# Optimization experiments

Hardware: AMD Instinct MI355X
Metric: run time of the kernel (lower is better)

Reference implementation:

```python
import jax, jax.numpy as jnp
import numpy as np
import math

NEIGHBOR_RADIUS = 30.0

def _masked_softmax(logits, mask, axis):
    # mask: bool, True = keep; all-masked rows return zeros
    p = jax.nn.softmax(jnp.where(mask, logits, -1e9), axis=axis) * mask.astype(logits.dtype)
    return p / jnp.clip(jnp.sum(p, axis=axis, keepdims=True), 1e-9, None)

def _forward(agents_state, agents_mask, map_polylines, map_poly_mask,
             map_poly_type, map_tl_status, map_on_route,
             pm_w1, pm_b1, pm_w2, pm_b2, type_emb, tl_emb, route_emb,
             mo_w1, mo_b1, mo_w2, mo_b2,
             ae_w1, ae_b1, ae_w2, ae_b2, ae_w3, ae_b3,
             mr_w1, mr_b1, mr_w2, mr_b2,
             nr_w1, nr_b1, nr_w2, nr_b2,
             to_w1, to_b1, to_w2, to_b2):
    relu = jax.nn.relu
    a_mask = (agents_mask > 0.5).astype(agents_state.dtype)   # (B,N,T)
    a_feat = agents_state[..., :5]
    # ---- map polyline node encoder ----
    h = relu(map_polylines @ pm_w1 + pm_b1)                   # (B,M,L,H)
    h = relu(h @ pm_w2 + pm_b2)
    h = h.max(axis=2)                                         # (B,M,H) max-pool over points
    t_idx = jnp.clip(map_poly_type, 0, type_emb.shape[0] - 1)
    s_idx = jnp.clip(map_tl_status, 0, tl_emb.shape[0] - 1)
    r_idx = jnp.clip(map_on_route, 0, route_emb.shape[0] - 1)
    h = h + type_emb[t_idx] + tl_emb[s_idx] + route_emb[r_idx]
    h = relu(h @ mo_w1 + mo_b1) @ mo_w2 + mo_b2
    map_mask = map_poly_mask > 0.5                            # (B,M) bool
    map_node = h * map_mask[..., None].astype(h.dtype)        # (B,M,D)
    map_center = map_polylines.mean(axis=2)                   # (B,M,2)
    # ---- agent state encoder ----
    a = relu(a_feat @ ae_w1 + ae_b1)
    a = relu(a @ ae_w2 + ae_b2)
    a_emb = (a @ ae_w3 + ae_b3) * a_mask[..., None]           # (B,N,T,D)
    D = a_emb.shape[-1]
    # ---- agent -> map attention ----
    agent_pos = a_feat[..., 0:2]
    rel = map_center[:, None, None, :, :] - agent_pos[:, :, :, None, :]  # (B,N,T,M,2)
    dist = jnp.linalg.norm(rel, axis=-1, keepdims=True)
    rel_feat = jnp.concatenate([rel, dist], axis=-1)          # (B,N,T,M,3)
    rel_score = (relu(rel_feat @ mr_w1 + mr_b1) @ mr_w2 + mr_b2)[..., 0]  # (B,N,T,M)
    dot = jnp.einsum('bntd,bmd->bntm', a_emb, map_node) / math.sqrt(D)
    score_mask = jnp.broadcast_to(map_mask[:, None, None, :], dot.shape)
    attn = _masked_softmax(dot + rel_score, score_mask, axis=-1)
    map_ctx = jnp.einsum('bntm,bmd->bntd', attn, map_node)    # (B,N,T,D)
    # ---- neighbor graph attention ----
    pos = a_feat[..., 0:2]
    vel = a_feat[..., 3:5]
    pos_j = jnp.transpose(pos, (0, 2, 1, 3))                  # (B,T,N,2)
    vel_j = jnp.transpose(vel, (0, 2, 1, 3))
    rel_pos = pos_j[:, None, :, :, :] - pos[:, :, :, None, :] # (B,N,T,N,2) = p_j - p_i
    rel_vel = vel_j[:, None, :, :, :] - vel[:, :, :, None, :]
    dist_ij = jnp.linalg.norm(rel_pos, axis=-1, keepdims=True)
    rel_ij = jnp.concatenate([rel_pos, rel_vel, dist_ij], axis=-1)        # (B,N,T,N,5)
    nbr_score = (relu(rel_ij @ nr_w1 + nr_b1) @ nr_w2 + nr_b2)[..., 0]    # (B,N,T,N)
    am_b = agents_mask > 0.5
    valid_i = am_b[..., None]                                 # (B,N,T,1)
    valid_j = jnp.transpose(am_b, (0, 2, 1))[:, None, :, :]   # (B,1,T,N)
    N = pos.shape[1]
    not_self = ~jnp.eye(N, dtype=bool)[None, :, None, :]      # (1,N,1,N)
    nbr_mask = valid_i & valid_j & (dist_ij[..., 0] <= NEIGHBOR_RADIUS) & not_self
    dot_n = jnp.einsum('bitd,bjtd->bitj', a_emb, a_emb) / math.sqrt(D)
    w_n = _masked_softmax(dot_n + nbr_score, nbr_mask, axis=-1)
    nbr_ctx = jnp.einsum('bitj,bjtd->bitd', w_n, a_emb)       # (B,N,T,D)
    # ---- tau head ----
    tau = jnp.concatenate([a_emb, map_ctx, nbr_ctx], axis=-1)
    tau = relu(tau @ to_w1 + to_b1) @ to_w2 + to_b2
    return tau * a_mask[..., None]

def setup_inputs() -> dict:
    key = jax.random.key(0)
    B, N, T, M, L = 2, 32, 32, 256, 20
    H, D, TAU = 128, 128, 64
    ks = jax.random.split(key, 32)
    def f(i, shp):
        return jax.random.normal(ks[i], shp, jnp.float32) * 0.05
    inp = {}
    inp['agents_state'] = jax.random.normal(ks[0], (B, N, T, 5), jnp.float32) * jnp.array([50., 50., 1., 5., 5.], jnp.float32)
    inp['agents_mask'] = jnp.ones((B, N, T), jnp.float32)
    inp['map_polylines'] = jax.random.normal(ks[1], (B, M, L, 2), jnp.float32) * 50.0
    inp['map_poly_mask'] = jnp.ones((B, M), jnp.float32)
    inp['map_poly_type'] = jax.random.randint(ks[2], (B, M), 0, 4)
    inp['map_tl_status'] = jax.random.randint(ks[3], (B, M), 0, 8)
    inp['map_on_route'] = jax.random.randint(ks[4], (B, M), 0, 2)
    inp['pm_w1'] = f(5, (2, H));  inp['pm_b1'] = jnp.zeros((H,), jnp.float32)
    inp['pm_w2'] = f(6, (H, H)); inp['pm_b2'] = jnp.zeros((H,), jnp.float32)
    inp['type_emb'] = f(7, (4, H)); inp['tl_emb'] = f(8, (8, H)); inp['route_emb'] = f(9, (2, H))
    inp['mo_w1'] = f(10, (H, H)); inp['mo_b1'] = jnp.zeros((H,), jnp.float32)
    inp['mo_w2'] = f(11, (H, D)); inp['mo_b2'] = jnp.zeros((D,), jnp.float32)
    inp['ae_w1'] = f(12, (5, H)); inp['ae_b1'] = jnp.zeros((H,), jnp.float32)
    inp['ae_w2'] = f(13, (H, H)); inp['ae_b2'] = jnp.zeros((H,), jnp.float32)
    inp['ae_w3'] = f(14, (H, D)); inp['ae_b3'] = jnp.zeros((D,), jnp.float32)
    inp['mr_w1'] = f(15, (3, H)); inp['mr_b1'] = jnp.zeros((H,), jnp.float32)
    inp['mr_w2'] = f(16, (H, 1)); inp['mr_b2'] = jnp.zeros((1,), jnp.float32)
    inp['nr_w1'] = f(17, (5, H)); inp['nr_b1'] = jnp.zeros((H,), jnp.float32)
    inp['nr_w2'] = f(18, (H, 1)); inp['nr_b2'] = jnp.zeros((1,), jnp.float32)
    inp['to_w1'] = f(19, (3 * D, H)); inp['to_b1'] = jnp.zeros((H,), jnp.float32)
    inp['to_w2'] = f(20, (H, TAU)); inp['to_b2'] = jnp.zeros((TAU,), jnp.float32)
    return inp

def reference(agents_state, agents_mask, map_polylines, map_poly_mask,
              map_poly_type, map_tl_status, map_on_route,
              pm_w1, pm_b1, pm_w2, pm_b2, type_emb, tl_emb, route_emb,
              mo_w1, mo_b1, mo_w2, mo_b2,
              ae_w1, ae_b1, ae_w2, ae_b2, ae_w3, ae_b3,
              mr_w1, mr_b1, mr_w2, mr_b2,
              nr_w1, nr_b1, nr_w2, nr_b2,
              to_w1, to_b1, to_w2, to_b2):
    return _forward(agents_state, agents_mask, map_polylines, map_poly_mask,
                    map_poly_type, map_tl_status, map_on_route,
                    pm_w1, pm_b1, pm_w2, pm_b2, type_emb, tl_emb, route_emb,
                    mo_w1, mo_b1, mo_w2, mo_b2,
                    ae_w1, ae_b1, ae_w2, ae_b2, ae_w3, ae_b3,
                    mr_w1, mr_b1, mr_w2, mr_b2,
                    nr_w1, nr_b1, nr_w2, nr_b2,
                    to_w1, to_b1, to_w2, to_b2)
```

## Files before the change

kernel.cpp:

```cpp
#include <hip/hip_runtime.h>
#include <hip/hip_bf16.h>

#define Bb 2
#define Nn 32
#define Tt 32
#define Mm 256
#define Ll 20
#define Hh 128
#define Dd 128
#define TAUu 64
#define RSQRT_D 0.08838834764831843f

__device__ __forceinline__ float rlane(float v, int l) {
    return __int_as_float(__builtin_amdgcn_readlane(__float_as_int(v), l));
}

__global__ __launch_bounds__(128) void k_map(
    const float* __restrict__ poly, const float* __restrict__ pmask,
    const int* __restrict__ ptype, const int* __restrict__ ptl, const int* __restrict__ proute,
    const float* __restrict__ pm_w1, const float* __restrict__ pm_b1,
    const float* __restrict__ pm_w2, const float* __restrict__ pm_b2,
    const float* __restrict__ type_emb, const float* __restrict__ tl_emb, const float* __restrict__ route_emb,
    const float* __restrict__ mo_w1, const float* __restrict__ mo_b1,
    const float* __restrict__ mo_w2, const float* __restrict__ mo_b2,
    float* __restrict__ map_node, float* __restrict__ map_nodeT, float* __restrict__ map_center)
{
    int bm = blockIdx.x;
    int b  = bm >> 8, m = bm & 255;
    int h  = threadIdx.x;
    int lam = h & 63, wv = h >> 6;
    int obase = ((wv ^ 1) << 6) + lam;
    __shared__ float xch[Ll][Hh];

    const float* pp = poly + bm * (Ll*2);
    float w1x = pm_w1[h], w1y = pm_w1[Hh+h], b1v = pm_b1[h];
    float h1r[Ll];
    #pragma unroll
    for (int l = 0; l < Ll; ++l) {
        float xl = pp[2*l], yl = pp[2*l+1];
        h1r[l] = fmaxf(fmaf(w1x, xl, fmaf(w1y, yl, b1v)), 0.f);
    }
    #pragma unroll
    for (int l = 0; l < Ll; ++l) xch[l][h] = h1r[l];
    __syncthreads();
    float lo[Ll], hi[Ll];
    #pragma unroll
    for (int l = 0; l < Ll; ++l) {
        float o = xch[l][obase];
        lo[l] = wv ? o : h1r[l];
        hi[l] = wv ? h1r[l] : o;
    }
    float b2v = pm_b2[h];
    float acc[Ll];
    #pragma unroll
    for (int l = 0; l < Ll; ++l) acc[l] = b2v;
    #pragma unroll
    for (int k = 0; k < 64; ++k) {
        float w = pm_w2[k*Hh + h];
        #pragma unroll
        for (int l = 0; l < Ll; ++l) acc[l] = fmaf(rlane(lo[l], k), w, acc[l]);
    }
    #pragma unroll
    for (int k = 0; k < 64; ++k) {
        float w = pm_w2[(64+k)*Hh + h];
        #pragma unroll
        for (int l = 0; l < Ll; ++l) acc[l] = fmaf(rlane(hi[l], k), w, acc[l]);
    }
    float mx = 0.f;
    #pragma unroll
    for (int l = 0; l < Ll; ++l) mx = fmaxf(mx, acc[l]);

    int ti = min(max(ptype[bm], 0), 3);
    int si = min(max(ptl[bm], 0), 7);
    int ri = min(max(proute[bm], 0), 1);
    float hval = mx + type_emb[ti*Hh+h] + tl_emb[si*Hh+h] + route_emb[ri*Hh+h];

    __syncthreads();
    xch[0][h] = hval;
    __syncthreads();
    {
        float o = xch[0][obase];
        float l1 = wv ? o : hval, h1 = wv ? hval : o;
        float a1 = mo_b1[h];
        #pragma unroll
        for (int k = 0; k < 64; ++k) a1 = fmaf(rlane(l1, k), mo_w1[k*Hh + h], a1);
        #pragma unroll
        for (int k = 0; k < 64; ++k) a1 = fmaf(rlane(h1, k), mo_w1[(64+k)*Hh + h], a1);
        hval = fmaxf(a1, 0.f);
    }
    __syncthreads();
    xch[0][h] = hval;
    __syncthreads();
    float val;
    {
        float o = xch[0][obase];
        float l1 = wv ? o : hval, h1 = wv ? hval : o;
        float a2 = mo_b2[h];
        #pragma unroll
        for (int k = 0; k < 64; ++k) a2 = fmaf(rlane(l1, k), mo_w2[k*Dd + h], a2);
        #pragma unroll
        for (int k = 0; k < 64; ++k) a2 = fmaf(rlane(h1, k), mo_w2[(64+k)*Dd + h], a2);
        val = a2;
    }
    float mk = (pmask[bm] > 0.5f) ? 1.f : 0.f;
    val *= mk;
    map_node[bm*Dd + h] = val;
    map_nodeT[(b*Dd + h)*Mm + m] = val;
    if (h == 0) {
        float sx = 0.f, sy = 0.f;
        #pragma unroll
        for (int l = 0; l < Ll; ++l) { sx += pp[2*l]; sy += pp[2*l+1]; }
        map_center[bm*2+0] = sx / (float)Ll;
        map_center[bm*2+1] = sy / (float)Ll;
    }
}

__global__ __launch_bounds__(128) void k_agent(
    const float* __restrict__ astate, const float* __restrict__ amask,
    const float* __restrict__ ae_w1, const float* __restrict__ ae_b1,
    const float* __restrict__ ae_w2, const float* __restrict__ ae_b2,
    const float* __restrict__ ae_w3, const float* __restrict__ ae_b3,
    float* __restrict__ a_emb)
{
    int r0 = blockIdx.x * 4;
    int h  = threadIdx.x;
    int lam = h & 63, wv = h >> 6;
    int obase = ((wv ^ 1) << 6) + lam;
    __shared__ float xch[4][Hh];

    float w1[5];
    #pragma unroll
    for (int k = 0; k < 5; ++k) w1[k] = ae_w1[k*Hh + h];
    float b1v = ae_b1[h];
    float a1[4];
    #pragma unroll
    for (int r = 0; r < 4; ++r) {
        const float* st = astate + (r0+r)*5;
        float a = b1v;
        #pragma unroll
        for (int k = 0; k < 5; ++k) a = fmaf(w1[k], st[k], a);
        a1[r] = fmaxf(a, 0.f);
    }
    #pragma unroll
    for (int r = 0; r < 4; ++r) xch[r][h] = a1[r];
    __syncthreads();
    float lo[4], hi[4];
    #pragma unroll
    for (int r = 0; r < 4; ++r) {
        float o = xch[r][obase];
        lo[r] = wv ? o : a1[r];
        hi[r] = wv ? a1[r] : o;
    }
    float b2v = ae_b2[h];
    float ac[4] = {b2v, b2v, b2v, b2v};
    #pragma unroll
    for (int k = 0; k < 64; ++k) {
        float w = ae_w2[k*Hh + h];
        #pragma unroll
        for (int r = 0; r < 4; ++r) ac[r] = fmaf(rlane(lo[r], k), w, ac[r]);
    }
    #pragma unroll
    for (int k = 0; k < 64; ++k) {
        float w = ae_w2[(64+k)*Hh + h];
        #pragma unroll
        for (int r = 0; r < 4; ++r) ac[r] = fmaf(rlane(hi[r], k), w, ac[r]);
    }
    #pragma unroll
    for (int r = 0; r < 4; ++r) a1[r] = fmaxf(ac[r], 0.f);
    __syncthreads();
    #pragma unroll
    for (int r = 0; r < 4; ++r) xch[r][h] = a1[r];
    __syncthreads();
    #pragma unroll
    for (int r = 0; r < 4; ++r) {
        float o = xch[r][obase];
        lo[r] = wv ? o : a1[r];
        hi[r] = wv ? a1[r] : o;
    }
    float b3v = ae_b3[h];
    #pragma unroll
    for (int r = 0; r < 4; ++r) ac[r] = b3v;
    #pragma unroll
    for (int k = 0; k < 64; ++k) {
        float w = ae_w3[k*Dd + h];
        #pragma unroll
        for (int r = 0; r < 4; ++r) ac[r] = fmaf(rlane(lo[r], k), w, ac[r]);
    }
    #pragma unroll
    for (int k = 0; k < 64; ++k) {
        float w = ae_w3[(64+k)*Dd + h];
        #pragma unroll
        for (int r = 0; r < 4; ++r) ac[r] = fmaf(rlane(hi[r], k), w, ac[r]);
    }
    #pragma unroll
    for (int r = 0; r < 4; ++r) {
        float mk = (amask[r0+r] > 0.5f) ? 1.f : 0.f;
        a_emb[(r0+r)*Dd + h] = ac[r] * mk;
    }
}

__global__ __launch_bounds__(256) void k_fused(
    const float* __restrict__ astate, const float* __restrict__ amask,
    const float* __restrict__ pmask,
    const float* __restrict__ a_emb, const float* __restrict__ map_node,
    const float* __restrict__ map_nodeT, const float* __restrict__ map_center,
    const float* __restrict__ mr_w1, const float* __restrict__ mr_b1,
    const float* __restrict__ mr_w2, const float* __restrict__ mr_b2,
    const float* __restrict__ nr_w1, const float* __restrict__ nr_b1,
    const float* __restrict__ nr_w2, const float* __restrict__ nr_b2,
    const float* __restrict__ to_w1, const float* __restrict__ to_b1,
    const float* __restrict__ to_w2, const float* __restrict__ to_b2,
    float* __restrict__ out)
{
    int r0 = blockIdx.x * 4;
    int b  = r0 >> 10;
    int i  = (r0 >> 5) & 31;
    int t0 = r0 & 31;
    int tid = threadIdx.x;
    int lam = tid & 63, wv = tid >> 6;

    __shared__ float tau[4][3*Dd];
    __shared__ float lg4[4][Mm];
    __shared__ float p4[Mm][4];
    __shared__ float ctxp[4][512];
    __shared__ float w1n_s[5*Hh];
    __shared__ float b1n_s[Hh];
    __shared__ float w2n_s[Hh];
    __shared__ float jd[4][Nn][5];
    __shared__ float lgn[4][Nn];
    __shared__ float p4n[Nn][4];
    __shared__ float g1s[4][Hh];

    for (int q = tid; q < 512; q += 256) tau[q>>7][q&127] = a_emb[(r0 + (q>>7))*Dd + (q&127)];
    for (int q = tid; q < 5*Hh; q += 256) w1n_s[q] = nr_w1[q];
    if (tid < Hh) { b1n_s[tid] = nr_b1[tid]; w2n_s[tid] = nr_w2[tid]; }
    if (tid < 128) {
        int rr = tid >> 5, j = tid & 31;
        int rj = (b*Nn + j)*Tt + t0 + rr;
        jd[rr][j][0] = astate[rj*5+0];
        jd[rr][j][1] = astate[rj*5+1];
        jd[rr][j][2] = astate[rj*5+3];
        jd[rr][j][3] = astate[rj*5+4];
        jd[rr][j][4] = amask[rj];
    }
    __syncthreads();

    {
        int m = tid;
        float cx = map_center[(b*Mm+m)*2+0];
        float cy = map_center[(b*Mm+m)*2+1];
        float rx[4], ry[4], dv[4], sA[4], dt[4];
        float b2c = mr_b2[0];
        #pragma unroll
        for (int r = 0; r < 4; ++r) {
            float px = astate[(r0+r)*5+0];
            float py = astate[(r0+r)*5+1];
            rx[r] = cx - px; ry[r] = cy - py;
            dv[r] = sqrtf(rx[r]*rx[r] + ry[r]*ry[r]);
            sA[r] = b2c; dt[r] = 0.f;
        }
        #pragma unroll 4
        for (int k = 0; k < Hh; ++k) {
            float wa = mr_w1[k], wb = mr_w1[Hh+k], wc = mr_w1[2*Hh+k];
            float bb = mr_b1[k], w2 = mr_w2[k];
            #pragma unroll
            for (int r = 0; r < 4; ++r) {
                float t1 = fmaf(rx[r], wa, fmaf(ry[r], wb, fmaf(dv[r], wc, bb)));
                t1 = fmaxf(t1, 0.f);
                sA[r] = fmaf(t1, w2, sA[r]);
            }
        }
        #pragma unroll 4
        for (int d = 0; d < Dd; ++d) {
            float v = map_nodeT[(b*Dd + d)*Mm + m];
            #pragma unroll
            for (int r = 0; r < 4; ++r)
                dt[r] = fmaf(v, a_emb[(r0+r)*Dd + d], dt[r]);
        }
        bool mk = pmask[b*Mm+m] > 0.5f;
        #pragma unroll
        for (int r = 0; r < 4; ++r)
            lg4[r][m] = mk ? fmaf(dt[r], RSQRT_D, sA[r]) : -1e30f;
    }
    __syncthreads();

    {
        float x0 = lg4[wv][lam], x1 = lg4[wv][64+lam], x2 = lg4[wv][128+lam], x3 = lg4[wv][192+lam];
        float mxv = fmaxf(fmaxf(x0,x1), fmaxf(x2,x3));
        for (int off = 32; off; off >>= 1) mxv = fmaxf(mxv, __shfl_xor(mxv, off));
        float e0 = (x0 > -1e29f) ? expf(x0-mxv) : 0.f;
        float e1 = (x1 > -1e29f) ? expf(x1-mxv) : 0.f;
        float e2 = (x2 > -1e29f) ? expf(x2-mxv) : 0.f;
        float e3 = (x3 > -1e29f) ? expf(x3-mxv) : 0.f;
        float sm = e0+e1+e2+e3;
        for (int off = 32; off; off >>= 1) sm += __shfl_xor(sm, off);
        float inv = 1.f / fmaxf(sm, 1e-9f);
        p4[lam][wv]     = e0*inv;
        p4[64+lam][wv]  = e1*inv;
        p4[128+lam][wv] = e2*inv;
        p4[192+lam][wv] = e3*inv;
    }
    __syncthreads();

    {
        int m0 = wv * 64;
        float4 pv = *(const float4*)&p4[m0 + lam][0];
        float pr0 = pv.x, pr1 = pv.y, pr2 = pv.z, pr3 = pv.w;
        float a00=0.f,a01=0.f,a10=0.f,a11=0.f,a20=0.f,a21=0.f,a30=0.f,a31=0.f;
        #pragma unroll
        for (int mm = 0; mm < 64; ++mm) {
            const float* np = map_node + (b*Mm + m0 + mm)*Dd;
            float v0 = np[lam], v1 = np[64+lam];
            float s0 = rlane(pr0, mm), s1 = rlane(pr1, mm), s2 = rlane(pr2, mm), s3 = rlane(pr3, mm);
            a00 = fmaf(s0, v0, a00); a01 = fmaf(s0, v1, a01);
            a10 = fmaf(s1, v0, a10); a11 = fmaf(s1, v1, a11);
            a20 = fmaf(s2, v0, a20); a21 = fmaf(s2, v1, a21);
            a30 = fmaf(s3, v0, a30); a31 = fmaf(s3, v1, a31);
        }
        ctxp[wv][0*Dd + lam] = a00; ctxp[wv][0*Dd + 64+lam] = a01;
        ctxp[wv][1*Dd + lam] = a10; ctxp[wv][1*Dd + 64+lam] = a11;
        ctxp[wv][2*Dd + lam] = a20; ctxp[wv][2*Dd + 64+lam] = a21;
        ctxp[wv][3*Dd + lam] = a30; ctxp[wv][3*Dd + 64+lam] = a31;
    }
    __syncthreads();
    for (int q = tid; q < 512; q += 256) {
        float s = ctxp[0][q] + ctxp[1][q] + ctxp[2][q] + ctxp[3][q];
        tau[q>>7][Dd + (q&127)] = s;
    }
    __syncthreads();

    {
        int j = tid >> 3, c = tid & 7;
        float b2c = nr_b2[0];
        float rpx[4], rpy[4], rvx[4], rvy[4], dd[4], am[4], ad[4];
        #pragma unroll
        for (int r = 0; r < 4; ++r) {
            float pxi = astate[(r0+r)*5+0], pyi = astate[(r0+r)*5+1];
            float vxi = astate[(r0+r)*5+3], vyi = astate[(r0+r)*5+4];
            rpx[r] = jd[r][j][0] - pxi; rpy[r] = jd[r][j][1] - pyi;
            rvx[r] = jd[r][j][2] - vxi; rvy[r] = jd[r][j][3] - vyi;
            dd[r]  = sqrtf(rpx[r]*rpx[r] + rpy[r]*rpy[r]);
            am[r] = 0.f; ad[r] = 0.f;
        }
        #pragma unroll
        for (int u = 0; u < 16; ++u) {
            int hh = (u<<3) + c;
            float wA = w1n_s[hh], wB = w1n_s[Hh+hh], wC = w1n_s[2*Hh+hh];
            float wD = w1n_s[3*Hh+hh], wE = w1n_s[4*Hh+hh];
            float bb = b1n_s[hh], w2 = w2n_s[hh];
            #pragma unroll
            for (int r = 0; r < 4; ++r) {
                float t1 = fmaf(rpx[r], wA, fmaf(rpy[r], wB, fmaf(rvx[r], wC,
                           fmaf(rvy[r], wD, fmaf(dd[r], wE, bb)))));
                t1 = fmaxf(t1, 0.f);
                am[r] = fmaf(t1, w2, am[r]);
                float ejv = a_emb[((size_t)((b*Nn + j)*Tt + t0 + r))*Dd + hh];
                ad[r] = fmaf(tau[r][hh], ejv, ad[r]);
            }
        }
        #pragma unroll
        for (int r = 0; r < 4; ++r) {
            am[r] += __shfl_xor(am[r], 1); ad[r] += __shfl_xor(ad[r], 1);
            am[r] += __shfl_xor(am[r], 2); ad[r] += __shfl_xor(ad[r], 2);
            am[r] += __shfl_xor(am[r], 4); ad[r] += __shfl_xor(ad[r], 4);
        }
        if (c == 0) {
            #pragma unroll
            for (int r = 0; r < 4; ++r) {
                bool vi = amask[r0+r] > 0.5f;
                bool vj = jd[r][j][4] > 0.5f;
                bool ok = vi && vj && (dd[r] <= 30.0f) && (j != i);
                lgn[r][j] = ok ? fmaf(ad[r], RSQRT_D, b2c + am[r]) : -1e30f;
            }
        }
    }
    __syncthreads();

    {
        float x = (lam < Nn) ? lgn[wv][lam] : -1e30f;
        float mxv = x;
        for (int off = 32; off; off >>= 1) mxv = fmaxf(mxv, __shfl_xor(mxv, off));
        float e = (x > -1e29f) ? expf(x - mxv) : 0.f;
        float sm = e;
        for (int off = 32; off; off >>= 1) sm += __shfl_xor(sm, off);
        float inv = 1.f / fmaxf(sm, 1e-9f);
        if (lam < Nn) p4n[lam][wv] = e * inv;
    }
    __syncthreads();

    {
        int d = tid & 127, hf = tid >> 7;
        float ac[4] = {0.f,0.f,0.f,0.f};
        #pragma unroll
        for (int jj = 0; jj < 16; ++jj) {
            int j2 = (hf<<4) + jj;
            float4 pv = *(const float4*)&p4n[j2][0];
            size_t base = (size_t)((b*Nn + j2)*Tt + t0);
            float v0 = a_emb[(base+0)*Dd + d];
            float v1 = a_emb[(base+1)*Dd + d];
            float v2 = a_emb[(base+2)*Dd + d];
            float v3 = a_emb[(base+3)*Dd + d];
            ac[0] = fmaf(pv.x, v0, ac[0]);
            ac[1] = fmaf(pv.y, v1, ac[1]);
            ac[2] = fmaf(pv.z, v2, ac[2]);
            ac[3] = fmaf(pv.w, v3, ac[3]);
        }
        if (hf == 1) {
            #pragma unroll
            for (int r = 0; r < 4; ++r) ctxp[0][r*Dd + d] = ac[r];
        }
        __syncthreads();
        if (hf == 0) {
            #pragma unroll
            for (int r = 0; r < 4; ++r) tau[r][2*Dd + d] = ac[r] + ctxp[0][r*Dd + d];
        }
    }
    __syncthreads();

    {
        int h = tid & 127, rp = tid >> 7;
        float ta[6], tb[6];
        #pragma unroll
        for (int c = 0; c < 6; ++c) {
            ta[c] = tau[rp][c*64 + lam];
            tb[c] = tau[rp+2][c*64 + lam];
        }
        float acc0 = 0.f, acc1 = 0.f;
        #pragma unroll
        for (int c = 0; c < 6; ++c) {
            #pragma unroll
            for (int kk = 0; kk < 64; ++kk) {
                float w = to_w1[(c*64+kk)*Hh + h];
                acc0 = fmaf(rlane(ta[c], kk), w, acc0);
                acc1 = fmaf(rlane(tb[c], kk), w, acc1);
            }
        }
        float bv = to_b1[h];
        g1s[rp][h]   = fmaxf(acc0 + bv, 0.f);
        g1s[rp+2][h] = fmaxf(acc1 + bv, 0.f);
    }
    __syncthreads();

    {
        float ga = g1s[wv][lam], gb = g1s[wv][64+lam];
        float acc = to_b2[lam];
        #pragma unroll
        for (int kk = 0; kk < 64; ++kk)
            acc = fmaf(rlane(ga, kk), to_w2[kk*TAUu + lam], acc);
        #pragma unroll
        for (int kk = 0; kk < 64; ++kk)
            acc = fmaf(rlane(gb, kk), to_w2[(64+kk)*TAUu + lam], acc);
        float mk = (amask[r0+wv] > 0.5f) ? 1.f : 0.f;
        out[(r0+wv)*TAUu + lam] = acc * mk;
    }
}

extern "C" void kernel_launch(void* const* d_in, const int* in_sizes, int n_in,
                              void* d_out, int out_size, void* d_ws, size_t ws_size,
                              hipStream_t stream) {
    const float* agents_state  = (const float*)d_in[0];
    const float* agents_mask   = (const float*)d_in[1];
    const float* map_polylines = (const float*)d_in[2];
    const float* map_poly_mask = (const float*)d_in[3];
    const int*   map_poly_type = (const int*)d_in[4];
    const int*   map_tl_status = (const int*)d_in[5];
    const int*   map_on_route  = (const int*)d_in[6];
    const float* pm_w1 = (const float*)d_in[7];
    const float* pm_b1 = (const float*)d_in[8];
    const float* pm_w2 = (const float*)d_in[9];
    const float* pm_b2 = (const float*)d_in[10];
    const float* type_emb  = (const float*)d_in[11];
    const float* tl_emb    = (const float*)d_in[12];
    const float* route_emb = (const float*)d_in[13];
    const float* mo_w1 = (const float*)d_in[14];
    const float* mo_b1 = (const float*)d_in[15];
    const float* mo_w2 = (const float*)d_in[16];
    const float* mo_b2 = (const float*)d_in[17];
    const float* ae_w1 = (const float*)d_in[18];
    const float* ae_b1 = (const float*)d_in[19];
    const float* ae_w2 = (const float*)d_in[20];
    const float* ae_b2 = (const float*)d_in[21];
    const float* ae_w3 = (const float*)d_in[22];
    const float* ae_b3 = (const float*)d_in[23];
    const float* mr_w1 = (const float*)d_in[24];
    const float* mr_b1 = (const float*)d_in[25];
    const float* mr_w2 = (const float*)d_in[26];
    const float* mr_b2 = (const float*)d_in[27];
    const float* nr_w1 = (const float*)d_in[28];
    const float* nr_b1 = (const float*)d_in[29];
    const float* nr_w2 = (const float*)d_in[30];
    const float* nr_b2 = (const float*)d_in[31];
    const float* to_w1 = (const float*)d_in[32];
    const float* to_b1 = (const float*)d_in[33];
    const float* to_w2 = (const float*)d_in[34];
    const float* to_b2 = (const float*)d_in[35];

    float* ws = (float*)d_ws;
    float* map_node   = ws;
    float* map_nodeT  = ws + 65536;
    float* map_center = ws + 131072;
    float* a_emb      = ws + 132096;

    float* out = (float*)d_out;

    k_map<<<Bb*Mm, 128, 0, stream>>>(map_polylines, map_poly_mask,
        map_poly_type, map_tl_status, map_on_route,
        pm_w1, pm_b1, pm_w2, pm_b2, type_emb, tl_emb, route_emb,
        mo_w1, mo_b1, mo_w2, mo_b2, map_node, map_nodeT, map_center);

    k_agent<<<Bb*Nn*Tt/4, 128, 0, stream>>>(agents_state, agents_mask,
        ae_w1, ae_b1, ae_w2, ae_b2, ae_w3, ae_b3, a_emb);

    k_fused<<<Bb*Nn*Tt/4, 256, 0, stream>>>(agents_state, agents_mask,
        map_poly_mask, a_emb, map_node, map_nodeT, map_center,
        mr_w1, mr_b1, mr_w2, mr_b2,
        nr_w1, nr_b1, nr_w2, nr_b2,
        to_w1, to_b1, to_w2, to_b2, out);
}
```

Before: 210.1 us.

## Restructure pipeline into three kernels with precomputed first-layer projections

Replaces the map/agent/fused kernel trio with three new kernels. The first merges the map and agent encoders into one launch and splits each K reduction across waves. The encoders now also precompute the linear parts of the relation MLPs (map-center and agent-position projections), plus transposed agent embeddings and position tables. The second kernel computes map and neighbor attention in separate block ranges, and the third runs the trajectory output MLP. The aim is to remove redundant per-pair first-layer work and raise parallelism, at the cost of more workspace traffic and an extra launch.

```diff
diff --git a/kernel.cpp b/kernel.cpp
--- a/kernel.cpp
+++ b/kernel.cpp
@@ -1,21 +1,12 @@
 #include <hip/hip_runtime.h>
-#include <hip/hip_bf16.h>
-
-#define Bb 2
-#define Nn 32
-#define Tt 32
-#define Mm 256
-#define Ll 20
-#define Hh 128
-#define Dd 128
-#define TAUu 64
+
 #define RSQRT_D 0.08838834764831843f
 
-__device__ __forceinline__ float rlane(float v, int l) {
+__device__ __forceinline__ float rl(float v, int l) {
     return __int_as_float(__builtin_amdgcn_readlane(__float_as_int(v), l));
 }
 
-__global__ __launch_bounds__(128) void k_map(
+__global__ __launch_bounds__(256) void k_p1(
     const float* __restrict__ poly, const float* __restrict__ pmask,
     const int* __restrict__ ptype, const int* __restrict__ ptl, const int* __restrict__ proute,
     const float* __restrict__ pm_w1, const float* __restrict__ pm_b1,
@@ -23,436 +14,432 @@
     const float* __restrict__ type_emb, const float* __restrict__ tl_emb, const float* __restrict__ route_emb,
     const float* __restrict__ mo_w1, const float* __restrict__ mo_b1,
     const float* __restrict__ mo_w2, const float* __restrict__ mo_b2,
-    float* __restrict__ map_node, float* __restrict__ map_nodeT, float* __restrict__ map_center)
-{
-    int bm = blockIdx.x;
-    int b  = bm >> 8, m = bm & 255;
-    int h  = threadIdx.x;
-    int lam = h & 63, wv = h >> 6;
-    int obase = ((wv ^ 1) << 6) + lam;
-    __shared__ float xch[Ll][Hh];
-
-    const float* pp = poly + bm * (Ll*2);
-    float w1x = pm_w1[h], w1y = pm_w1[Hh+h], b1v = pm_b1[h];
-    float h1r[Ll];
-    #pragma unroll
-    for (int l = 0; l < Ll; ++l) {
-        float xl = pp[2*l], yl = pp[2*l+1];
-        h1r[l] = fmaxf(fmaf(w1x, xl, fmaf(w1y, yl, b1v)), 0.f);
-    }
-    #pragma unroll
-    for (int l = 0; l < Ll; ++l) xch[l][h] = h1r[l];
-    __syncthreads();
-    float lo[Ll], hi[Ll];
-    #pragma unroll
-    for (int l = 0; l < Ll; ++l) {
-        float o = xch[l][obase];
-        lo[l] = wv ? o : h1r[l];
-        hi[l] = wv ? h1r[l] : o;
-    }
-    float b2v = pm_b2[h];
-    float acc[Ll];
-    #pragma unroll
-    for (int l = 0; l < Ll; ++l) acc[l] = b2v;
-    #pragma unroll
-    for (int k = 0; k < 64; ++k) {
-        float w = pm_w2[k*Hh + h];
-        #pragma unroll
-        for (int l = 0; l < Ll; ++l) acc[l] = fmaf(rlane(lo[l], k), w, acc[l]);
-    }
-    #pragma unroll
-    for (int k = 0; k < 64; ++k) {
-        float w = pm_w2[(64+k)*Hh + h];
-        #pragma unroll
-        for (int l = 0; l < Ll; ++l) acc[l] = fmaf(rlane(hi[l], k), w, acc[l]);
-    }
-    float mx = 0.f;
-    #pragma unroll
-    for (int l = 0; l < Ll; ++l) mx = fmaxf(mx, acc[l]);
-
-    int ti = min(max(ptype[bm], 0), 3);
-    int si = min(max(ptl[bm], 0), 7);
-    int ri = min(max(proute[bm], 0), 1);
-    float hval = mx + type_emb[ti*Hh+h] + tl_emb[si*Hh+h] + route_emb[ri*Hh+h];
-
-    __syncthreads();
-    xch[0][h] = hval;
-    __syncthreads();
-    {
-        float o = xch[0][obase];
-        float l1 = wv ? o : hval, h1 = wv ? hval : o;
-        float a1 = mo_b1[h];
-        #pragma unroll
-        for (int k = 0; k < 64; ++k) a1 = fmaf(rlane(l1, k), mo_w1[k*Hh + h], a1);
-        #pragma unroll
-        for (int k = 0; k < 64; ++k) a1 = fmaf(rlane(h1, k), mo_w1[(64+k)*Hh + h], a1);
-        hval = fmaxf(a1, 0.f);
-    }
-    __syncthreads();
-    xch[0][h] = hval;
-    __syncthreads();
-    float val;
-    {
-        float o = xch[0][obase];
-        float l1 = wv ? o : hval, h1 = wv ? hval : o;
-        float a2 = mo_b2[h];
-        #pragma unroll
-        for (int k = 0; k < 64; ++k) a2 = fmaf(rlane(l1, k), mo_w2[k*Dd + h], a2);
-        #pragma unroll
-        for (int k = 0; k < 64; ++k) a2 = fmaf(rlane(h1, k), mo_w2[(64+k)*Dd + h], a2);
-        val = a2;
-    }
-    float mk = (pmask[bm] > 0.5f) ? 1.f : 0.f;
-    val *= mk;
-    map_node[bm*Dd + h] = val;
-    map_nodeT[(b*Dd + h)*Mm + m] = val;
-    if (h == 0) {
-        float sx = 0.f, sy = 0.f;
-        #pragma unroll
-        for (int l = 0; l < Ll; ++l) { sx += pp[2*l]; sy += pp[2*l+1]; }
-        map_center[bm*2+0] = sx / (float)Ll;
-        map_center[bm*2+1] = sy / (float)Ll;
-    }
-}
-
-__global__ __launch_bounds__(128) void k_agent(
+    const float* __restrict__ mr_w1, const float* __restrict__ mr_b1,
     const float* __restrict__ astate, const float* __restrict__ amask,
     const float* __restrict__ ae_w1, const float* __restrict__ ae_b1,
     const float* __restrict__ ae_w2, const float* __restrict__ ae_b2,
     const float* __restrict__ ae_w3, const float* __restrict__ ae_b3,
-    float* __restrict__ a_emb)
+    const float* __restrict__ nr_w1, const float* __restrict__ nr_b1,
+    float* __restrict__ map_node, float* __restrict__ map_nodeT,
+    float* __restrict__ cm, float* __restrict__ center,
+    float* __restrict__ a_emb, float* __restrict__ aT,
+    float* __restrict__ q2, float* __restrict__ qn, float* __restrict__ posT)
 {
-    int r0 = blockIdx.x * 4;
-    int h  = threadIdx.x;
-    int lam = h & 63, wv = h >> 6;
-    int obase = ((wv ^ 1) << 6) + lam;
-    __shared__ float xch[4][Hh];
-
-    float w1[5];
-    #pragma unroll
-    for (int k = 0; k < 5; ++k) w1[k] = ae_w1[k*Hh + h];
-    float b1v = ae_b1[h];
-    float a1[4];
-    #pragma unroll
-    for (int r = 0; r < 4; ++r) {
-        const float* st = astate + (r0+r)*5;
-        float a = b1v;
-        #pragma unroll
-        for (int k = 0; k < 5; ++k) a = fmaf(w1[k], st[k], a);
-        a1[r] = fmaxf(a, 0.f);
-    }
-    #pragma unroll
-    for (int r = 0; r < 4; ++r) xch[r][h] = a1[r];
-    __syncthreads();
-    float lo[4], hi[4];
-    #pragma unroll
-    for (int r = 0; r < 4; ++r) {
-        float o = xch[r][obase];
-        lo[r] = wv ? o : a1[r];
-        hi[r] = wv ? a1[r] : o;
-    }
-    float b2v = ae_b2[h];
-    float ac[4] = {b2v, b2v, b2v, b2v};
-    #pragma unroll
-    for (int k = 0; k < 64; ++k) {
-        float w = ae_w2[k*Hh + h];
-        #pragma unroll
-        for (int r = 0; r < 4; ++r) ac[r] = fmaf(rlane(lo[r], k), w, ac[r]);
-    }
-    #pragma unroll
-    for (int k = 0; k < 64; ++k) {
-        float w = ae_w2[(64+k)*Hh + h];
-        #pragma unroll
-        for (int r = 0; r < 4; ++r) ac[r] = fmaf(rlane(hi[r], k), w, ac[r]);
-    }
-    #pragma unroll
-    for (int r = 0; r < 4; ++r) a1[r] = fmaxf(ac[r], 0.f);
-    __syncthreads();
-    #pragma unroll
-    for (int r = 0; r < 4; ++r) xch[r][h] = a1[r];
-    __syncthreads();
-    #pragma unroll
-    for (int r = 0; r < 4; ++r) {
-        float o = xch[r][obase];
-        lo[r] = wv ? o : a1[r];
-        hi[r] = wv ? a1[r] : o;
-    }
-    float b3v = ae_b3[h];
-    #pragma unroll
-    for (int r = 0; r < 4; ++r) ac[r] = b3v;
-    #pragma unroll
-    for (int k = 0; k < 64; ++k) {
-        float w = ae_w3[k*Dd + h];
-        #pragma unroll
-        for (int r = 0; r < 4; ++r) ac[r] = fmaf(rlane(lo[r], k), w, ac[r]);
-    }
-    #pragma unroll
-    for (int k = 0; k < 64; ++k) {
-        float w = ae_w3[(64+k)*Dd + h];
-        #pragma unroll
-        for (int r = 0; r < 4; ++r) ac[r] = fmaf(rlane(hi[r], k), w, ac[r]);
-    }
-    #pragma unroll
-    for (int r = 0; r < 4; ++r) {
-        float mk = (amask[r0+r] > 0.5f) ? 1.f : 0.f;
-        a_emb[(r0+r)*Dd + h] = ac[r] * mk;
+    int tid = threadIdx.x;
+    int lam = tid & 63;
+    __shared__ float red[20][128];
+    __shared__ float xch[128];
+
+    if (blockIdx.x < 512) {
+        int bm = blockIdx.x;
+        int b = bm >> 8, m = bm & 255;
+        int h = tid & 127, lp = tid >> 7;
+        int pidx = bm*40 + lam; if (pidx > 20479) pidx = 20479;
+        float ptreg = poly[pidx];
+        int x = lp*64 + lam;
+        float w1x = pm_w1[x], w1y = pm_w1[128+x], b1v = pm_b1[x];
+        float h1r[20];
+        #pragma unroll
+        for (int l = 0; l < 20; ++l) {
+            float xl = rl(ptreg, 2*l), yl = rl(ptreg, 2*l+1);
+            h1r[l] = fmaxf(fmaf(w1x, xl, fmaf(w1y, yl, b1v)), 0.f);
+        }
+        float acc[20];
+        #pragma unroll
+        for (int l = 0; l < 20; ++l) acc[l] = 0.f;
+        #pragma unroll
+        for (int kk = 0; kk < 64; ++kk) {
+            float w = pm_w2[(lp*64+kk)*128 + h];
+            #pragma unroll
+            for (int l = 0; l < 20; ++l) acc[l] = fmaf(rl(h1r[l], kk), w, acc[l]);
+        }
+        if (lp == 1) {
+            #pragma unroll
+            for (int l = 0; l < 20; ++l) red[l][h] = acc[l];
+        }
+        __syncthreads();
+        if (lp == 0) {
+            float mx = -1e30f;
+            #pragma unroll
+            for (int l = 0; l < 20; ++l) mx = fmaxf(mx, acc[l] + red[l][h]);
+            mx = fmaxf(mx + pm_b2[h], 0.f);
+            int ti = min(max(ptype[bm],0),3);
+            int si = min(max(ptl[bm],0),7);
+            int ri = min(max(proute[bm],0),1);
+            xch[h] = mx + type_emb[ti*128+h] + tl_emb[si*128+h] + route_emb[ri*128+h];
+        }
+        __syncthreads();
+        float src = xch[lp*64 + lam];
+        float a1p = 0.f;
+        #pragma unroll
+        for (int kk = 0; kk < 64; ++kk)
+            a1p = fmaf(rl(src, kk), mo_w1[(lp*64+kk)*128 + h], a1p);
+        if (lp == 1) red[0][h] = a1p;
+        __syncthreads();
+        if (lp == 0) {
+            float a1v = fmaxf(a1p + red[0][h] + mo_b1[h], 0.f);
+            red[1][h] = a1v;
+        }
+        __syncthreads();
+        float src2 = red[1][lp*64 + lam];
+        float a2p = 0.f;
+        #pragma unroll
+        for (int kk = 0; kk < 64; ++kk)
+            a2p = fmaf(rl(src2, kk), mo_w2[(lp*64+kk)*128 + h], a2p);
+        if (lp == 1) red[2][h] = a2p;
+        __syncthreads();
+        float sx = 0.f, sy = 0.f;
+        #pragma unroll
+        for (int l = 0; l < 20; ++l) { sx += rl(ptreg, 2*l); sy += rl(ptreg, 2*l+1); }
+        sx *= 0.05f; sy *= 0.05f;
+        if (lp == 0) {
+            float val = a2p + red[2][h] + mo_b2[h];
+            float mk = (pmask[bm] > 0.5f) ? 1.f : 0.f;
+            val *= mk;
+            map_node[bm*128 + h] = val;
+            map_nodeT[(b*128+h)*256 + m] = val;
+            cm[(b*128+h)*256 + m] = fmaf(sx, mr_w1[h], fmaf(sy, mr_w1[128+h], mr_b1[h]));
+            if (h == 0) { center[bm*2+0] = sx; center[bm*2+1] = sy; }
+        }
+    } else {
+        int qw = (blockIdx.x - 512)*4 + (tid >> 6);
+        int r0b = qw * 4;
+        int aidx = r0b*5 + lam; if (aidx > 10239) aidx = 10239;
+        float streg = astate[aidx];
+        float w1l[5], w1h[5];
+        #pragma unroll
+        for (int c = 0; c < 5; ++c) { w1l[c] = ae_w1[c*128+lam]; w1h[c] = ae_w1[c*128+64+lam]; }
+        float b1l = ae_b1[lam], b1h = ae_b1[64+lam];
+        float a1lo[4], a1hi[4];
+        #pragma unroll
+        for (int r = 0; r < 4; ++r) {
+            float px = rl(streg, r*5+0), py = rl(streg, r*5+1), pz = rl(streg, r*5+2);
+            float vx = rl(streg, r*5+3), vy = rl(streg, r*5+4);
+            float lo = b1l, hi = b1h;
+            lo = fmaf(px,w1l[0],lo); hi = fmaf(px,w1h[0],hi);
+            lo = fmaf(py,w1l[1],lo); hi = fmaf(py,w1h[1],hi);
+            lo = fmaf(pz,w1l[2],lo); hi = fmaf(pz,w1h[2],hi);
+            lo = fmaf(vx,w1l[3],lo); hi = fmaf(vx,w1h[3],hi);
+            lo = fmaf(vy,w1l[4],lo); hi = fmaf(vy,w1h[4],hi);
+            a1lo[r] = fmaxf(lo, 0.f); a1hi[r] = fmaxf(hi, 0.f);
+        }
+        float c0[4], c1[4];
+        {
+            float b2l = ae_b2[lam], b2h = ae_b2[64+lam];
+            #pragma unroll
+            for (int r = 0; r < 4; ++r) { c0[r] = b2l; c1[r] = b2h; }
+        }
+        #pragma unroll
+        for (int k = 0; k < 64; ++k) {
+            float wl = ae_w2[k*128+lam], wh = ae_w2[k*128+64+lam];
+            #pragma unroll
+            for (int r = 0; r < 4; ++r) { float xv = rl(a1lo[r], k); c0[r]=fmaf(xv,wl,c0[r]); c1[r]=fmaf(xv,wh,c1[r]); }
+        }
+        #pragma unroll
+        for (int k = 0; k < 64; ++k) {
+            float wl = ae_w2[(64+k)*128+lam], wh = ae_w2[(64+k)*128+64+lam];
+            #pragma unroll
+            for (int r = 0; r < 4; ++r) { float xv = rl(a1hi[r], k); c0[r]=fmaf(xv,wl,c0[r]); c1[r]=fmaf(xv,wh,c1[r]); }
+        }
+        #pragma unroll
+        for (int r = 0; r < 4; ++r) { a1lo[r] = fmaxf(c0[r],0.f); a1hi[r] = fmaxf(c1[r],0.f); }
+        {
+            float b3l = ae_b3[lam], b3h = ae_b3[64+lam];
+            #pragma unroll
+            for (int r = 0; r < 4; ++r) { c0[r] = b3l; c1[r] = b3h; }
+        }
+        #pragma unroll
+        for (int k = 0; k < 64; ++k) {
+            float wl = ae_w3[k*128+lam], wh = ae_w3[k*128+64+lam];
+            #pragma unroll
+            for (int r = 0; r < 4; ++r) { float xv = rl(a1lo[r], k); c0[r]=fmaf(xv,wl,c0[r]); c1[r]=fmaf(xv,wh,c1[r]); }
+        }
+        #pragma unroll
+        for (int k = 0; k < 64; ++k) {
+            float wl = ae_w3[(64+k)*128+lam], wh = ae_w3[(64+k)*128+64+lam];
+            #pragma unroll
+            for (int r = 0; r < 4; ++r) { float xv = rl(a1hi[r], k); c0[r]=fmaf(xv,wl,c0[r]); c1[r]=fmaf(xv,wh,c1[r]); }
+        }
+        float nA_l = nr_w1[lam],     nA_h = nr_w1[64+lam];
+        float nB_l = nr_w1[128+lam], nB_h = nr_w1[192+lam];
+        float nC_l = nr_w1[256+lam], nC_h = nr_w1[320+lam];
+        float nD_l = nr_w1[384+lam], nD_h = nr_w1[448+lam];
+        float nb_l = nr_b1[lam],     nb_h = nr_b1[64+lam];
+        #pragma unroll
+        for (int r = 0; r < 4; ++r) {
+            int rr = r0b + r;
+            float mk = (amask[rr] > 0.5f) ? 1.f : 0.f;
+            float e0 = c0[r]*mk, e1 = c1[r]*mk;
+            int bb = rr >> 10, nn = (rr >> 5) & 31, tt = rr & 31;
+            int bt = bb*32 + tt;
+            a_emb[rr*128 + lam]    = e0;
+            a_emb[rr*128 + 64+lam] = e1;
+            aT[(bt*128 + lam)*32 + nn]    = e0;
+            aT[(bt*128 + 64+lam)*32 + nn] = e1;
+            float px = rl(streg, r*5+0), py = rl(streg, r*5+1);
+            float vx = rl(streg, r*5+3), vy = rl(streg, r*5+4);
+            float ql = fmaf(px,nA_l,fmaf(py,nB_l,fmaf(vx,nC_l, vy*nD_l)));
+            float qh = fmaf(px,nA_h,fmaf(py,nB_h,fmaf(vx,nC_h, vy*nD_h)));
+            qn[rr*128 + lam]    = ql;
+            qn[rr*128 + 64+lam] = qh;
+            q2[(bt*128 + lam)*32 + nn]    = ql + nb_l;
+            q2[(bt*128 + 64+lam)*32 + nn] = qh + nb_h;
+            if (lam == 0) {
+                posT[(bt*5+0)*32+nn] = px;
+                posT[(bt*5+1)*32+nn] = py;
+                posT[(bt*5+2)*32+nn] = vx;
+                posT[(bt*5+3)*32+nn] = vy;
+                posT[(bt*5+4)*32+nn] = amask[rr];
+            }
+        }
     }
 }
 
-__global__ __launch_bounds__(256) void k_fused(
-    const float* __restrict__ astate, const float* __restrict__ amask,
-    const float* __restrict__ pmask,
+__global__ __launch_bounds__(256) void k_p2(
+    const float* __restrict__ astate, const float* __restrict__ pmask,
     const float* __restrict__ a_emb, const float* __restrict__ map_node,
-    const float* __restrict__ map_nodeT, const float* __restrict__ map_center,
-    const float* __restrict__ mr_w1, const float* __restrict__ mr_b1,
-    const float* __restrict__ mr_w2, const float* __restrict__ mr_b2,
-    const float* __restrict__ nr_w1, const float* __restrict__ nr_b1,
-    const float* __restrict__ nr_w2, const float* __restrict__ nr_b2,
+    const float* __restrict__ map_nodeT, const float* __restrict__ center,
+    const float* __restrict__ cm,
+    const float* __restrict__ mr_w1, const float* __restrict__ mr_w2, const float* __restrict__ mr_b2,
+    const float* __restrict__ qn, const float* __restrict__ q2,
+    const float* __restrict__ aT, const float* __restrict__ posT,
+    const float* __restrict__ nr_w1, const float* __restrict__ nr_w2, const float* __restrict__ nr_b2,
+    float* __restrict__ map_ctx, float* __restrict__ p_n)
+{
+    int tid = threadIdx.x;
+    int lam = tid & 63, wv = tid >> 6;
+    __shared__ float lg4[4][256];
+    __shared__ __align__(16) float p4[256*4];
+    __shared__ float ctxp[4][512];
+
+    if (blockIdx.x < 512) {
+        int r0 = blockIdx.x * 4;
+        int b = r0 >> 10;
+        int m = tid;
+        int aidx = r0*5 + lam; if (aidx > 10239) aidx = 10239;
+        float streg = astate[aidx];
+        float wa_l = mr_w1[lam],     wa_h = mr_w1[64+lam];
+        float wb_l = mr_w1[128+lam], wb_h = mr_w1[192+lam];
+        float wc_l = mr_w1[256+lam], wc_h = mr_w1[320+lam];
+        float w2_l = mr_w2[lam],     w2_h = mr_w2[64+lam];
+        float b2c = mr_b2[0];
+        float cx = center[(b*256+m)*2+0], cy = center[(b*256+m)*2+1];
+        float prl[4], prh[4], eal[4], eah[4], dd[4], dt[4], sA[4];
+        #pragma unroll
+        for (int r = 0; r < 4; ++r) {
+            float px = rl(streg, r*5+0), py = rl(streg, r*5+1);
+            prl[r] = fmaf(px, wa_l, py*wb_l);
+            prh[r] = fmaf(px, wa_h, py*wb_h);
+            eal[r] = a_emb[(r0+r)*128 + lam];
+            eah[r] = a_emb[(r0+r)*128 + 64+lam];
+            float rx = cx - px, ry = cy - py;
+            dd[r] = sqrtf(rx*rx + ry*ry);
+            dt[r] = 0.f; sA[r] = b2c;
+        }
+        const float* mT  = map_nodeT + b*128*256 + m;
+        const float* cmp = cm        + b*128*256 + m;
+        #pragma unroll
+        for (int d = 0; d < 64; ++d) {
+            float v = mT[d*256];
+            #pragma unroll
+            for (int r = 0; r < 4; ++r) dt[r] = fmaf(v, rl(eal[r], d), dt[r]);
+        }
+        #pragma unroll
+        for (int d = 0; d < 64; ++d) {
+            float v = mT[(64+d)*256];
+            #pragma unroll
+            for (int r = 0; r < 4; ++r) dt[r] = fmaf(v, rl(eah[r], d), dt[r]);
+        }
+        #pragma unroll
+        for (int hh = 0; hh < 64; ++hh) {
+            float cmv = cmp[hh*256];
+            float wcv = rl(wc_l, hh), w2v = rl(w2_l, hh);
+            #pragma unroll
+            for (int r = 0; r < 4; ++r) {
+                float t1 = fmaf(dd[r], wcv, cmv - rl(prl[r], hh));
+                sA[r] = fmaf(fmaxf(t1, 0.f), w2v, sA[r]);
+            }
+        }
+        #pragma unroll
+        for (int hh = 0; hh < 64; ++hh) {
+            float cmv = cmp[(64+hh)*256];
+            float wcv = rl(wc_h, hh), w2v = rl(w2_h, hh);
+            #pragma unroll
+            for (int r = 0; r < 4; ++r) {
+                float t1 = fmaf(dd[r], wcv, cmv - rl(prh[r], hh));
+                sA[r] = fmaf(fmaxf(t1, 0.f), w2v, sA[r]);
+            }
+        }
+        bool mk = pmask[b*256+m] > 0.5f;
+        #pragma unroll
+        for (int r = 0; r < 4; ++r)
+            lg4[r][m] = mk ? fmaf(dt[r], RSQRT_D, sA[r]) : -1e30f;
+        __syncthreads();
+        {
+            float x0 = lg4[wv][lam], x1 = lg4[wv][64+lam], x2 = lg4[wv][128+lam], x3 = lg4[wv][192+lam];
+            float mxv = fmaxf(fmaxf(x0,x1), fmaxf(x2,x3));
+            #pragma unroll
+            for (int off = 32; off; off >>= 1) mxv = fmaxf(mxv, __shfl_xor(mxv, off));
+            float e0 = (x0 > -1e29f) ? expf(x0-mxv) : 0.f;
+            float e1 = (x1 > -1e29f) ? expf(x1-mxv) : 0.f;
+            float e2 = (x2 > -1e29f) ? expf(x2-mxv) : 0.f;
+            float e3 = (x3 > -1e29f) ? expf(x3-mxv) : 0.f;
+            float sm = e0+e1+e2+e3;
+            #pragma unroll
+            for (int off = 32; off; off >>= 1) sm += __shfl_xor(sm, off);
+            float inv = 1.f / fmaxf(sm, 1e-9f);
+            p4[(lam)*4     + wv] = e0*inv;
+            p4[(64+lam)*4  + wv] = e1*inv;
+            p4[(128+lam)*4 + wv] = e2*inv;
+            p4[(192+lam)*4 + wv] = e3*inv;
+        }
+        __syncthreads();
+        {
+            int m0 = wv*64;
+            float4 pq = *(const float4*)&p4[(m0+lam)*4];
+            float a0[4] = {0.f,0.f,0.f,0.f}, a1[4] = {0.f,0.f,0.f,0.f};
+            const float* mn = map_node + (b*256 + m0)*128;
+            #pragma unroll
+            for (int mm = 0; mm < 64; ++mm) {
+                float v0 = mn[mm*128 + lam], v1 = mn[mm*128 + 64+lam];
+                float pp0 = rl(pq.x, mm), pp1 = rl(pq.y, mm), pp2 = rl(pq.z, mm), pp3 = rl(pq.w, mm);
+                a0[0]=fmaf(pp0,v0,a0[0]); a1[0]=fmaf(pp0,v1,a1[0]);
+                a0[1]=fmaf(pp1,v0,a0[1]); a1[1]=fmaf(pp1,v1,a1[1]);
+                a0[2]=fmaf(pp2,v0,a0[2]); a1[2]=fmaf(pp2,v1,a1[2]);
+                a0[3]=fmaf(pp3,v0,a0[3]); a1[3]=fmaf(pp3,v1,a1[3]);
+            }
+            #pragma unroll
+            for (int r = 0; r < 4; ++r) { ctxp[wv][r*128+lam] = a0[r]; ctxp[wv][r*128+64+lam] = a1[r]; }
+        }
+        __syncthreads();
+        for (int q = tid; q < 512; q += 256) {
+            float s = ctxp[0][q] + ctxp[1][q] + ctxp[2][q] + ctxp[3][q];
+            map_ctx[(r0 + (q>>7))*128 + (q & 127)] = s;
+        }
+    } else {
+        int beta = blockIdx.x - 512;
+        int r0 = beta*8 + wv*2;
+        int hf = lam >> 5, j = lam & 31;
+        bool hfb = (hf == 1);
+        int rr = r0 + hf;
+        int b = rr >> 10, ii = (rr >> 5) & 31, tt = rr & 31;
+        int bt = b*32 + tt;
+        float uqA_l = qn[r0*128+lam],     uqA_h = qn[r0*128+64+lam];
+        float uqB_l = qn[(r0+1)*128+lam], uqB_h = qn[(r0+1)*128+64+lam];
+        float eiA_l = a_emb[r0*128+lam],     eiA_h = a_emb[r0*128+64+lam];
+        float eiB_l = a_emb[(r0+1)*128+lam], eiB_h = a_emb[(r0+1)*128+64+lam];
+        float wE_l = nr_w1[512+lam], wE_h = nr_w1[576+lam];
+        float w2_l = nr_w2[lam],     w2_h = nr_w2[64+lam];
+        float pxj = posT[(bt*5+0)*32 + j];
+        float pyj = posT[(bt*5+1)*32 + j];
+        float vxj = posT[(bt*5+2)*32 + j];
+        float vyj = posT[(bt*5+3)*32 + j];
+        float mj  = posT[(bt*5+4)*32 + j];
+        float pxi = hfb ? rl(pxj, 32+ii) : rl(pxj, ii);
+        float pyi = hfb ? rl(pyj, 32+ii) : rl(pyj, ii);
+        float vxi = hfb ? rl(vxj, 32+ii) : rl(vxj, ii);
+        float vyi = hfb ? rl(vyj, 32+ii) : rl(vyj, ii);
+        float mi  = hfb ? rl(mj, 32+ii)  : rl(mj, ii);
+        float rpx = pxj-pxi, rpy = pyj-pyi;
+        float ddv = sqrtf(rpx*rpx + rpy*rpy);
+        (void)vxi; (void)vyi;
+        float s = nr_b2[0], dot = 0.f;
+        const float* q2p = q2 + bt*128*32 + j;
+        const float* aTp = aT + bt*128*32 + j;
+        #pragma unroll
+        for (int hh = 0; hh < 64; ++hh) {
+            float qjv = q2p[hh*32];
+            float ajv = aTp[hh*32];
+            float qiv = hfb ? rl(uqB_l, hh) : rl(uqA_l, hh);
+            float eiv = hfb ? rl(eiB_l, hh) : rl(eiA_l, hh);
+            float t1 = fmaf(ddv, rl(wE_l, hh), qjv - qiv);
+            s = fmaf(fmaxf(t1, 0.f), rl(w2_l, hh), s);
+            dot = fmaf(eiv, ajv, dot);
+        }
+        #pragma unroll
+        for (int hh = 0; hh < 64; ++hh) {
+            float qjv = q2p[(64+hh)*32];
+            float ajv = aTp[(64+hh)*32];
+            float qiv = hfb ? rl(uqB_h, hh) : rl(uqA_h, hh);
+            float eiv = hfb ? rl(eiB_h, hh) : rl(eiA_h, hh);
+            float t1 = fmaf(ddv, rl(wE_h, hh), qjv - qiv);
+            s = fmaf(fmaxf(t1, 0.f), rl(w2_h, hh), s);
+            dot = fmaf(eiv, ajv, dot);
+        }
+        bool ok = (mi > 0.5f) && (mj > 0.5f) && (ddv <= 30.0f) && (j != ii);
+        float lg = ok ? fmaf(dot, RSQRT_D, s) : -1e30f;
+        float mxv = lg;
+        #pragma unroll
+        for (int off = 16; off; off >>= 1) mxv = fmaxf(mxv, __shfl_xor(mxv, off));
+        float e = (lg > -1e29f) ? expf(lg - mxv) : 0.f;
+        float sm = e;
+        #pragma unroll
+        for (int off = 16; off; off >>= 1) sm += __shfl_xor(sm, off);
+        p_n[rr*32 + j] = e / fmaxf(sm, 1e-9f);
+    }
+}
+
+__global__ __launch_bounds__(256) void k_p3(
+    const float* __restrict__ amask, const float* __restrict__ a_emb,
+    const float* __restrict__ map_ctx, const float* __restrict__ p_n,
     const float* __restrict__ to_w1, const float* __restrict__ to_b1,
     const float* __restrict__ to_w2, const float* __restrict__ to_b2,
     float* __restrict__ out)
 {
-    int r0 = blockIdx.x * 4;
-    int b  = r0 >> 10;
-    int i  = (r0 >> 5) & 31;
-    int t0 = r0 & 31;
-    int tid = threadIdx.x;
-    int lam = tid & 63, wv = tid >> 6;
-
-    __shared__ float tau[4][3*Dd];
-    __shared__ float lg4[4][Mm];
-    __shared__ float p4[Mm][4];
-    __shared__ float ctxp[4][512];
-    __shared__ float w1n_s[5*Hh];
-    __shared__ float b1n_s[Hh];
-    __shared__ float w2n_s[Hh];
-    __shared__ float jd[4][Nn][5];
-    __shared__ float lgn[4][Nn];
-    __shared__ float p4n[Nn][4];
-    __shared__ float g1s[4][Hh];
-
-    for (int q = tid; q < 512; q += 256) tau[q>>7][q&127] = a_emb[(r0 + (q>>7))*Dd + (q&127)];
-    for (int q = tid; q < 5*Hh; q += 256) w1n_s[q] = nr_w1[q];
-    if (tid < Hh) { b1n_s[tid] = nr_b1[tid]; w2n_s[tid] = nr_w2[tid]; }
-    if (tid < 128) {
-        int rr = tid >> 5, j = tid & 31;
-        int rj = (b*Nn + j)*Tt + t0 + rr;
-        jd[rr][j][0] = astate[rj*5+0];
-        jd[rr][j][1] = astate[rj*5+1];
-        jd[rr][j][2] = astate[rj*5+3];
-        jd[rr][j][3] = astate[rj*5+4];
-        jd[rr][j][4] = amask[rj];
+    int tid = threadIdx.x, lam = tid & 63, wv = tid >> 6;
+    int r0 = blockIdx.x*8 + wv*2;
+    int b = r0 >> 10, t = r0 & 31;
+    float preg = p_n[r0*32 + lam];
+    float ncA0 = 0.f, ncA1 = 0.f, ncB0 = 0.f, ncB1 = 0.f;
+    #pragma unroll
+    for (int j = 0; j < 32; ++j) {
+        const float* ejA = a_emb + (((b*32+j)*32 + t))*128;
+        const float* ejB = ejA + 128;
+        float pA = rl(preg, j), pB = rl(preg, 32+j);
+        ncA0 = fmaf(pA, ejA[lam],    ncA0);
+        ncA1 = fmaf(pA, ejA[64+lam], ncA1);
+        ncB0 = fmaf(pB, ejB[lam],    ncB0);
+        ncB1 = fmaf(pB, ejB[64+lam], ncB1);
     }
-    __syncthreads();
-
-    {
-        int m = tid;
-        float cx = map_center[(b*Mm+m)*2+0];
-        float cy = map_center[(b*Mm+m)*2+1];
-        float rx[4], ry[4], dv[4], sA[4], dt[4];
-        float b2c = mr_b2[0];
-        #pragma unroll
-        for (int r = 0; r < 4; ++r) {
-            float px = astate[(r0+r)*5+0];
-            float py = astate[(r0+r)*5+1];
-            rx[r] = cx - px; ry[r] = cy - py;
-            dv[r] = sqrtf(rx[r]*rx[r] + ry[r]*ry[r]);
-            sA[r] = b2c; dt[r] = 0.f;
-        }
-        #pragma unroll 4
-        for (int k = 0; k < Hh; ++k) {
-            float wa = mr_w1[k], wb = mr_w1[Hh+k], wc = mr_w1[2*Hh+k];
-            float bb = mr_b1[k], w2 = mr_w2[k];
-            #pragma unroll
-            for (int r = 0; r < 4; ++r) {
-                float t1 = fmaf(rx[r], wa, fmaf(ry[r], wb, fmaf(dv[r], wc, bb)));
-                t1 = fmaxf(t1, 0.f);
-                sA[r] = fmaf(t1, w2, sA[r]);
-            }
-        }
-        #pragma unroll 4
-        for (int d = 0; d < Dd; ++d) {
-            float v = map_nodeT[(b*Dd + d)*Mm + m];
-            #pragma unroll
-            for (int r = 0; r < 4; ++r)
-                dt[r] = fmaf(v, a_emb[(r0+r)*Dd + d], dt[r]);
-        }
-        bool mk = pmask[b*Mm+m] > 0.5f;
-        #pragma unroll
-        for (int r = 0; r < 4; ++r)
-            lg4[r][m] = mk ? fmaf(dt[r], RSQRT_D, sA[r]) : -1e30f;
+    float tA[6], tB[6];
+    tA[0] = a_emb[r0*128+lam];       tA[1] = a_emb[r0*128+64+lam];
+    tA[2] = map_ctx[r0*128+lam];     tA[3] = map_ctx[r0*128+64+lam];
+    tA[4] = ncA0;                    tA[5] = ncA1;
+    tB[0] = a_emb[(r0+1)*128+lam];   tB[1] = a_emb[(r0+1)*128+64+lam];
+    tB[2] = map_ctx[(r0+1)*128+lam]; tB[3] = map_ctx[(r0+1)*128+64+lam];
+    tB[4] = ncB0;                    tB[5] = ncB1;
+    float gA0 = to_b1[lam], gA1 = to_b1[64+lam];
+    float gB0 = gA0, gB1 = gA1;
+    #pragma unroll
+    for (int c = 0; c < 6; ++c) {
+        #pragma unroll
+        for (int k = 0; k < 64; ++k) {
+            float w0 = to_w1[(c*64+k)*128 + lam];
+            float w1v = to_w1[(c*64+k)*128 + 64+lam];
+            float xA = rl(tA[c], k), xB = rl(tB[c], k);
+            gA0 = fmaf(xA, w0, gA0); gA1 = fmaf(xA, w1v, gA1);
+            gB0 = fmaf(xB, w0, gB0); gB1 = fmaf(xB, w1v, gB1);
+        }
     }
-    __syncthreads();
-
-    {
-        float x0 = lg4[wv][lam], x1 = lg4[wv][64+lam], x2 = lg4[wv][128+lam], x3 = lg4[wv][192+lam];
-        float mxv = fmaxf(fmaxf(x0,x1), fmaxf(x2,x3));
-        for (int off = 32; off; off >>= 1) mxv = fmaxf(mxv, __shfl_xor(mxv, off));
-        float e0 = (x0 > -1e29f) ? expf(x0-mxv) : 0.f;
-        float e1 = (x1 > -1e29f) ? expf(x1-mxv) : 0.f;
-        float e2 = (x2 > -1e29f) ? expf(x2-mxv) : 0.f;
-        float e3 = (x3 > -1e29f) ? expf(x3-mxv) : 0.f;
-        float sm = e0+e1+e2+e3;
-        for (int off = 32; off; off >>= 1) sm += __shfl_xor(sm, off);
-        float inv = 1.f / fmaxf(sm, 1e-9f);
-        p4[lam][wv]     = e0*inv;
-        p4[64+lam][wv]  = e1*inv;
-        p4[128+lam][wv] = e2*inv;
-        p4[192+lam][wv] = e3*inv;
+    gA0 = fmaxf(gA0, 0.f); gA1 = fmaxf(gA1, 0.f);
+    gB0 = fmaxf(gB0, 0.f); gB1 = fmaxf(gB1, 0.f);
+    float oA = to_b2[lam], oB = oA;
+    #pragma unroll
+    for (int k = 0; k < 64; ++k) {
+        float w = to_w2[k*64 + lam];
+        oA = fmaf(rl(gA0, k), w, oA);
+        oB = fmaf(rl(gB0, k), w, oB);
     }
-    __syncthreads();
-
-    {
-        int m0 = wv * 64;
-        float4 pv = *(const float4*)&p4[m0 + lam][0];
-        float pr0 = pv.x, pr1 = pv.y, pr2 = pv.z, pr3 = pv.w;
-        float a00=0.f,a01=0.f,a10=0.f,a11=0.f,a20=0.f,a21=0.f,a30=0.f,a31=0.f;
-        #pragma unroll
-        for (int mm = 0; mm < 64; ++mm) {
-            const float* np = map_node + (b*Mm + m0 + mm)*Dd;
-            float v0 = np[lam], v1 = np[64+lam];
-            float s0 = rlane(pr0, mm), s1 = rlane(pr1, mm), s2 = rlane(pr2, mm), s3 = rlane(pr3, mm);
-            a00 = fmaf(s0, v0, a00); a01 = fmaf(s0, v1, a01);
-            a10 = fmaf(s1, v0, a10); a11 = fmaf(s1, v1, a11);
-            a20 = fmaf(s2, v0, a20); a21 = fmaf(s2, v1, a21);
-            a30 = fmaf(s3, v0, a30); a31 = fmaf(s3, v1, a31);
-        }
-        ctxp[wv][0*Dd + lam] = a00; ctxp[wv][0*Dd + 64+lam] = a01;
-        ctxp[wv][1*Dd + lam] = a10; ctxp[wv][1*Dd + 64+lam] = a11;
-        ctxp[wv][2*Dd + lam] = a20; ctxp[wv][2*Dd + 64+lam] = a21;
-        ctxp[wv][3*Dd + lam] = a30; ctxp[wv][3*Dd + 64+lam] = a31;
+    #pragma unroll
+    for (int k = 0; k < 64; ++k) {
+        float w = to_w2[(64+k)*64 + lam];
+        oA = fmaf(rl(gA1, k), w, oA);
+        oB = fmaf(rl(gB1, k), w, oB);
     }
-    __syncthreads();
-    for (int q = tid; q < 512; q += 256) {
-        float s = ctxp[0][q] + ctxp[1][q] + ctxp[2][q] + ctxp[3][q];
-        tau[q>>7][Dd + (q&127)] = s;
-    }
-    __syncthreads();
-
-    {
-        int j = tid >> 3, c = tid & 7;
-        float b2c = nr_b2[0];
-        float rpx[4], rpy[4], rvx[4], rvy[4], dd[4], am[4], ad[4];
-        #pragma unroll
-        for (int r = 0; r < 4; ++r) {
-            float pxi = astate[(r0+r)*5+0], pyi = astate[(r0+r)*5+1];
-            float vxi = astate[(r0+r)*5+3], vyi = astate[(r0+r)*5+4];
-            rpx[r] = jd[r][j][0] - pxi; rpy[r] = jd[r][j][1] - pyi;
-            rvx[r] = jd[r][j][2] - vxi; rvy[r] = jd[r][j][3] - vyi;
-            dd[r]  = sqrtf(rpx[r]*rpx[r] + rpy[r]*rpy[r]);
-            am[r] = 0.f; ad[r] = 0.f;
-        }
-        #pragma unroll
-        for (int u = 0; u < 16; ++u) {
-            int hh = (u<<3) + c;
-            float wA = w1n_s[hh], wB = w1n_s[Hh+hh], wC = w1n_s[2*Hh+hh];
-            float wD = w1n_s[3*Hh+hh], wE = w1n_s[4*Hh+hh];
-            float bb = b1n_s[hh], w2 = w2n_s[hh];
-            #pragma unroll
-            for (int r = 0; r < 4; ++r) {
-                float t1 = fmaf(rpx[r], wA, fmaf(rpy[r], wB, fmaf(rvx[r], wC,
-                           fmaf(rvy[r], wD, fmaf(dd[r], wE, bb)))));
-                t1 = fmaxf(t1, 0.f);
-                am[r] = fmaf(t1, w2, am[r]);
-                float ejv = a_emb[((size_t)((b*Nn + j)*Tt + t0 + r))*Dd + hh];
-                ad[r] = fmaf(tau[r][hh], ejv, ad[r]);
-            }
-        }
-        #pragma unroll
-        for (int r = 0; r < 4; ++r) {
-            am[r] += __shfl_xor(am[r], 1); ad[r] += __shfl_xor(ad[r], 1);
-            am[r] += __shfl_xor(am[r], 2); ad[r] += __shfl_xor(ad[r], 2);
-            am[r] += __shfl_xor(am[r], 4); ad[r] += __shfl_xor(ad[r], 4);
-        }
-        if (c == 0) {
-            #pragma unroll
-            for (int r = 0; r < 4; ++r) {
-                bool vi = amask[r0+r] > 0.5f;
-                bool vj = jd[r][j][4] > 0.5f;
-                bool ok = vi && vj && (dd[r] <= 30.0f) && (j != i);
-                lgn[r][j] = ok ? fmaf(ad[r], RSQRT_D, b2c + am[r]) : -1e30f;
-            }
-        }
-    }
-    __syncthreads();
-
-    {
-        float x = (lam < Nn) ? lgn[wv][lam] : -1e30f;
-        float mxv = x;
-        for (int off = 32; off; off >>= 1) mxv = fmaxf(mxv, __shfl_xor(mxv, off));
-        float e = (x > -1e29f) ? expf(x - mxv) : 0.f;
-        float sm = e;
-        for (int off = 32; off; off >>= 1) sm += __shfl_xor(sm, off);
-        float inv = 1.f / fmaxf(sm, 1e-9f);
-        if (lam < Nn) p4n[lam][wv] = e * inv;
-    }
-    __syncthreads();
-
-    {
-        int d = tid & 127, hf = tid >> 7;
-        float ac[4] = {0.f,0.f,0.f,0.f};
-        #pragma unroll
-        for (int jj = 0; jj < 16; ++jj) {
-            int j2 = (hf<<4) + jj;
-            float4 pv = *(const float4*)&p4n[j2][0];
-            size_t base = (size_t)((b*Nn + j2)*Tt + t0);
-            float v0 = a_emb[(base+0)*Dd + d];
-            float v1 = a_emb[(base+1)*Dd + d];
-            float v2 = a_emb[(base+2)*Dd + d];
-            float v3 = a_emb[(base+3)*Dd + d];
-            ac[0] = fmaf(pv.x, v0, ac[0]);
-            ac[1] = fmaf(pv.y, v1, ac[1]);
-            ac[2] = fmaf(pv.z, v2, ac[2]);
-            ac[3] = fmaf(pv.w, v3, ac[3]);
-        }
-        if (hf == 1) {
-            #pragma unroll
-            for (int r = 0; r < 4; ++r) ctxp[0][r*Dd + d] = ac[r];
-        }
-        __syncthreads();
-        if (hf == 0) {
-            #pragma unroll
-            for (int r = 0; r < 4; ++r) tau[r][2*Dd + d] = ac[r] + ctxp[0][r*Dd + d];
-        }
-    }
-    __syncthreads();
-
-    {
-        int h = tid & 127, rp = tid >> 7;
-        float ta[6], tb[6];
-        #pragma unroll
-        for (int c = 0; c < 6; ++c) {
-            ta[c] = tau[rp][c*64 + lam];
-            tb[c] = tau[rp+2][c*64 + lam];
-        }
-        float acc0 = 0.f, acc1 = 0.f;
-        #pragma unroll
-        for (int c = 0; c < 6; ++c) {
-            #pragma unroll
-            for (int kk = 0; kk < 64; ++kk) {
-                float w = to_w1[(c*64+kk)*Hh + h];
-                acc0 = fmaf(rlane(ta[c], kk), w, acc0);
-                acc1 = fmaf(rlane(tb[c], kk), w, acc1);
-            }
-        }
-        float bv = to_b1[h];
-        g1s[rp][h]   = fmaxf(acc0 + bv, 0.f);
-        g1s[rp+2][h] = fmaxf(acc1 + bv, 0.f);
-    }
-    __syncthreads();
-
-    {
-        float ga = g1s[wv][lam], gb = g1s[wv][64+lam];
-        float acc = to_b2[lam];
-        #pragma unroll
-        for (int kk = 0; kk < 64; ++kk)
-            acc = fmaf(rlane(ga, kk), to_w2[kk*TAUu + lam], acc);
-        #pragma unroll
-        for (int kk = 0; kk < 64; ++kk)
-            acc = fmaf(rlane(gb, kk), to_w2[(64+kk)*TAUu + lam], acc);
-        float mk = (amask[r0+wv] > 0.5f) ? 1.f : 0.f;
-        out[(r0+wv)*TAUu + lam] = acc * mk;
-    }
+    float mkA = (amask[r0]   > 0.5f) ? 1.f : 0.f;
+    float mkB = (amask[r0+1] > 0.5f) ? 1.f : 0.f;
+    out[r0*64     + lam] = oA * mkA;
+    out[(r0+1)*64 + lam] = oB * mkB;
 }
 
 extern "C" void kernel_launch(void* const* d_in, const int* in_sizes, int n_in,
@@ -496,24 +483,35 @@
     const float* to_b2 = (const float*)d_in[35];
 
     float* ws = (float*)d_ws;
-    float* map_node   = ws;
-    float* map_nodeT  = ws + 65536;
-    float* map_center = ws + 131072;
-    float* a_emb      = ws + 132096;
+    float* map_node  = ws;
+    float* map_nodeT = ws + 65536;
+    float* cm        = ws + 131072;
+    float* center    = ws + 196608;
+    float* a_emb     = ws + 197632;
+    float* aT        = ws + 459776;
+    float* q2        = ws + 721920;
+    float* qn        = ws + 984064;
+    float* posT      = ws + 1246208;
+    float* map_ctx   = ws + 1256448;
+    float* p_n       = ws + 1518592;
 
     float* out = (float*)d_out;
 
-    k_map<<<Bb*Mm, 128, 0, stream>>>(map_polylines, map_poly_mask,
+    k_p1<<<640, 256, 0, stream>>>(map_polylines, map_poly_mask,
         map_poly_type, map_tl_status, map_on_route,
         pm_w1, pm_b1, pm_w2, pm_b2, type_emb, tl_emb, route_emb,
-        mo_w1, mo_b1, mo_w2, mo_b2, map_node, map_nodeT, map_center);
-
-    k_agent<<<Bb*Nn*Tt/4, 128, 0, stream>>>(agents_state, agents_mask,
-        ae_w1, ae_b1, ae_w2, ae_b2, ae_w3, ae_b3, a_emb);
-
-    k_fused<<<Bb*Nn*Tt/4, 256, 0, stream>>>(agents_state, agents_mask,
-        map_poly_mask, a_emb, map_node, map_nodeT, map_center,
-        mr_w1, mr_b1, mr_w2, mr_b2,
-        nr_w1, nr_b1, nr_w2, nr_b2,
+        mo_w1, mo_b1, mo_w2, mo_b2, mr_w1, mr_b1,
+        agents_state, agents_mask,
+        ae_w1, ae_b1, ae_w2, ae_b2, ae_w3, ae_b3,
+        nr_w1, nr_b1,
+        map_node, map_nodeT, cm, center, a_emb, aT, q2, qn, posT);
+
+    k_p2<<<768, 256, 0, stream>>>(agents_state, map_poly_mask,
+        a_emb, map_node, map_nodeT, center, cm,
+        mr_w1, mr_w2, mr_b2,
+        qn, q2, aT, posT, nr_w1, nr_w2, nr_b2,
+        map_ctx, p_n);
+
+    k_p3<<<256, 256, 0, stream>>>(agents_mask, a_emb, map_ctx, p_n,
         to_w1, to_b1, to_w2, to_b2, out);
 }
```

New measurement: 303.9 us. 44.7% more time.
